# Performance work log

Hardware: AMD Instinct MI355X
Metric: run time of the kernel (lower is better)

The kernel has to match this reference:

```python
import jax, jax.numpy as jnp
import numpy as np

L, B, C_IN, C_OUT, C_COND, K, RATIO, TEMP = 1024, 8, 1024, 1024, 256, 4, 4, 30.0
HID = C_COND // RATIO


def setup_inputs() -> dict:
    key = jax.random.key(0)
    ks = jax.random.split(key, 8)
    s_in = 1.0 / np.sqrt(C_IN)
    s_cond = 1.0 / np.sqrt(C_COND)
    s_hid = 1.0 / np.sqrt(HID)
    return {
        "x": jax.random.normal(ks[0], (L, B, C_IN), jnp.float32),
        "cond": jax.random.normal(ks[1], (B, C_COND), jnp.float32),
        "fc1_w": jax.random.normal(ks[2], (HID, C_COND), jnp.float32) * s_cond,
        "fc1_b": jnp.zeros((HID,), jnp.float32),
        "fc2_w": jax.random.normal(ks[3], (K, HID), jnp.float32) * s_hid,
        "fc2_b": jnp.zeros((K,), jnp.float32),
        "weight": jax.random.normal(ks[4], (K, C_OUT, C_IN), jnp.float32) * s_in,
        "bias": jax.random.normal(ks[5], (K, C_OUT), jnp.float32) * s_in,
    }


def reference(x, cond, fc1_w, fc1_b, fc2_w, fc2_b, weight, bias):
    # attention over K experts, conditioned on style vector: (B, K)
    h = jax.nn.relu(cond @ fc1_w.T + fc1_b)
    att = jax.nn.softmax((h @ fc2_w.T + fc2_b) / TEMP, axis=-1)
    # per-sample aggregated weights: (B, C_out, C_in) and bias (B, C_out)
    w_b = jnp.einsum("bk,koi->boi", att, weight)
    b_b = att @ bias
    # grouped 1x1 conv == per-sample linear over the L dim: (L, B, C_out)
    out = jnp.einsum("lbi,boi->lbo", x, w_b) + b_b[None, :, :]
    return out
```

## Files before the change

### kernel.cpp

```cpp
#include <hip/hip_runtime.h>
#include <stdint.h>

#define L_DIM 1024
#define B_DIM 8
#define CIN   1024
#define COUT  1024
#define CCOND 256
#define KEXP  4
#define HID_DIM 64
#define TEMP_INV (1.0f/30.0f)

typedef float  f32x4 __attribute__((ext_vector_type(4)));
typedef __bf16 bf16x8 __attribute__((ext_vector_type(8)));

__device__ __forceinline__ ushort f2bf(float f) {
  union { float f; uint32_t u; } a; a.f = f;
  return (ushort)((a.u + 0x7fffu + ((a.u >> 16) & 1u)) >> 16);
}

__global__ __launch_bounds__(256) void prep_kernel(
                            const float* __restrict__ x,
                            const float* __restrict__ cond,
                            const float* __restrict__ fc1_w,
                            const float* __restrict__ fc1_b,
                            const float* __restrict__ fc2_w,
                            const float* __restrict__ fc2_b,
                            const float* __restrict__ bias,
                            ushort* __restrict__ xt,
                            float* __restrict__ att_out,
                            float* __restrict__ bb_out) {
  const int t = threadIdx.x;
  if (blockIdx.x == 0) {
    __shared__ float wlds[HID_DIM][CCOND + 4];
    __shared__ float clds[B_DIM][CCOND];
    __shared__ float h[B_DIM][HID_DIM];
    __shared__ float att[B_DIM][KEXP];
    #pragma unroll
    for (int ci = 0; ci < 16; ++ci) {
      int gi = ci * 256 + t;
      f32x4 v = ((const f32x4*)fc1_w)[gi];
      int j = gi >> 6, c4 = gi & 63;
      *(f32x4*)&wlds[j][c4 * 4] = v;
    }
    #pragma unroll
    for (int ci = 0; ci < 2; ++ci) {
      int gi = ci * 256 + t;
      ((f32x4*)clds)[gi] = ((const f32x4*)cond)[gi];
    }
    __syncthreads();
    {
      const int j = t & 63, b0 = t >> 6;
      float a0 = 0.f, a1 = 0.f;
      #pragma unroll 8
      for (int c4 = 0; c4 < 64; ++c4) {
        f32x4 wv = *(const f32x4*)&wlds[j][c4 * 4];
        f32x4 ca = *(const f32x4*)&clds[b0][c4 * 4];
        f32x4 cb = *(const f32x4*)&clds[b0 + 4][c4 * 4];
        a0 += wv.x*ca.x + wv.y*ca.y + wv.z*ca.z + wv.w*ca.w;
        a1 += wv.x*cb.x + wv.y*cb.y + wv.z*cb.z + wv.w*cb.w;
      }
      float bj = fc1_b[j];
      h[b0][j]     = fmaxf(a0 + bj, 0.0f);
      h[b0 + 4][j] = fmaxf(a1 + bj, 0.0f);
    }
    __syncthreads();
    if (t < B_DIM * KEXP) {
      const int b = t >> 2, k = t & 3;
      const float* wp = fc2_w + k * HID_DIM;
      float s = fc2_b[k];
      #pragma unroll 8
      for (int j = 0; j < HID_DIM; ++j) s = fmaf(h[b][j], wp[j], s);
      att[b][k] = s * TEMP_INV;
    }
    __syncthreads();
    if (t < B_DIM) {
      const int b = t;
      float m = fmaxf(fmaxf(att[b][0], att[b][1]), fmaxf(att[b][2], att[b][3]));
      float e0 = expf(att[b][0] - m), e1 = expf(att[b][1] - m);
      float e2 = expf(att[b][2] - m), e3 = expf(att[b][3] - m);
      float inv = 1.0f / (e0 + e1 + e2 + e3);
      att[b][0] = e0 * inv; att[b][1] = e1 * inv;
      att[b][2] = e2 * inv; att[b][3] = e3 * inv;
      att_out[b*KEXP+0] = att[b][0]; att_out[b*KEXP+1] = att[b][1];
      att_out[b*KEXP+2] = att[b][2]; att_out[b*KEXP+3] = att[b][3];
    }
    __syncthreads();
    for (int idx = t; idx < B_DIM * COUT; idx += 256) {
      const int b = idx >> 10, o = idx & (COUT - 1);
      float s = att[b][0] * bias[o]        + att[b][1] * bias[COUT + o]
              + att[b][2] * bias[2*COUT+o] + att[b][3] * bias[3*COUT+o];
      bb_out[idx] = s;
    }
  } else {
    const int C4 = CIN / 4;
    const int r0 = (blockIdx.x - 1) * 8;
    const f32x4* xp = (const f32x4*)x;
    f32x4 v[8];
    #pragma unroll
    for (int i = 0; i < 8; ++i)
      v[i] = xp[(size_t)(r0 + i) * C4 + t];
    #pragma unroll
    for (int i = 0; i < 8; ++i) {
      const int r = r0 + i;
      const int b = r & (B_DIM - 1);
      const int l = r >> 3;
      ushort4 o;
      o.x = f2bf(v[i].x); o.y = f2bf(v[i].y); o.z = f2bf(v[i].z); o.w = f2bf(v[i].w);
      ((ushort4*)xt)[(b * L_DIM + l) * C4 + t] = o;
    }
  }
}

__global__ void wmix_kernel(const float* __restrict__ weight,
                            const float* __restrict__ att,
                            ushort* __restrict__ wbb) {
  __shared__ float satt[B_DIM * KEXP];
  if (threadIdx.x < B_DIM * KEXP) satt[threadIdx.x] = att[threadIdx.x];
  __syncthreads();
  const int total4 = COUT * CIN / 4;
  int idx = blockIdx.x * blockDim.x + threadIdx.x;
  if (idx >= total4) return;
  f32x4 w0 = ((const f32x4*)weight)[idx];
  f32x4 w1 = ((const f32x4*)weight)[total4 + idx];
  f32x4 w2 = ((const f32x4*)weight)[2 * total4 + idx];
  f32x4 w3 = ((const f32x4*)weight)[3 * total4 + idx];
  #pragma unroll
  for (int b = 0; b < B_DIM; ++b) {
    f32x4 s = satt[b*4+0] * w0 + satt[b*4+1] * w1 + satt[b*4+2] * w2 + satt[b*4+3] * w3;
    ushort4 o;
    o.x = f2bf(s.x); o.y = f2bf(s.y); o.z = f2bf(s.z); o.w = f2bf(s.w);
    ((ushort4*)wbb)[b * total4 + idx] = o;
  }
}

#define GBM 256
#define GBN 128
#define GBK 64
#define GKT (CIN / GBK)

__global__ __launch_bounds__(512, 1) void gemm_kernel(
    const ushort* __restrict__ xt,
    const ushort* __restrict__ wbb,
    const float* __restrict__ bb,
    float* __restrict__ out)
{
  __shared__ ushort lds[3][(GBM + GBN) * GBK];

  const int bid = blockIdx.x;
  const int b  = bid & 7;
  const int tl = bid >> 3;
  const int mt = tl >> 3;
  const int nt = tl & 7;

  const int t = threadIdx.x;
  const int lane = t & 63;
  const int wid = t >> 6;
  const int wm = wid >> 1;
  const int wn = wid & 1;

  const ushort* __restrict__ Ag = xt  + (b * L_DIM + mt * GBM) * CIN;
  const ushort* __restrict__ Bg = wbb + (b * COUT  + nt * GBN) * CIN;

  const int srow = t >> 3;
  const int sg = (t & 7) ^ (srow & 7);

  f32x4 acc[4][4] = {};

  auto stage = [&](int bf, int kt) {
    #pragma unroll
    for (int i = 0; i < 4; ++i) {
      const int r = i * 64 + srow;
      __builtin_amdgcn_global_load_lds(
        (const __attribute__((address_space(1))) uint32_t*)(Ag + r * CIN + kt * GBK + sg * 8),
        (__attribute__((address_space(3))) uint32_t*)(&lds[bf][i * 4096 + t * 8]), 16, 0, 0);
    }
    #pragma unroll
    for (int i = 0; i < 2; ++i) {
      const int r = i * 64 + srow;
      __builtin_amdgcn_global_load_lds(
        (const __attribute__((address_space(1))) uint32_t*)(Bg + r * CIN + kt * GBK + sg * 8),
        (__attribute__((address_space(3))) uint32_t*)(&lds[bf][GBM * GBK + i * 4096 + t * 8]), 16, 0, 0);
    }
  };

  stage(0, 0);
  stage(1, 1);

  const int kg = lane >> 4;
  const int rr = lane & 15;

  #pragma unroll
  for (int kt = 0; kt < GKT; ++kt) {
    if (kt < GKT - 1) { asm volatile("s_waitcnt vmcnt(6)" ::: "memory"); }
    else              { asm volatile("s_waitcnt vmcnt(0)" ::: "memory"); }
    __builtin_amdgcn_sched_barrier(0);
    __builtin_amdgcn_s_barrier();
    __builtin_amdgcn_sched_barrier(0);
    if (kt + 2 < GKT) stage((kt + 2) % 3, kt + 2);
    __builtin_amdgcn_sched_barrier(0);

    const ushort* Ab = &lds[kt % 3][0];
    const ushort* Bb = &lds[kt % 3][GBM * GBK];
    bf16x8 af[4][2], bfv[4][2];
    #pragma unroll
    for (int kk = 0; kk < 2; ++kk) {
      const int sl = ((kk << 2) | kg) ^ (rr & 7);
      #pragma unroll
      for (int m = 0; m < 4; ++m)
        af[m][kk] = *(const bf16x8*)(Ab + (wm * 64 + m * 16 + rr) * GBK + sl * 8);
      #pragma unroll
      for (int n = 0; n < 4; ++n)
        bfv[n][kk] = *(const bf16x8*)(Bb + (wn * 64 + n * 16 + rr) * GBK + sl * 8);
    }
    __builtin_amdgcn_s_setprio(1);
    #pragma unroll
    for (int kk = 0; kk < 2; ++kk)
      #pragma unroll
      for (int m = 0; m < 4; ++m)
        #pragma unroll
        for (int n = 0; n < 4; ++n)
          acc[m][n] = __builtin_amdgcn_mfma_f32_16x16x32_bf16(af[m][kk], bfv[n][kk], acc[m][n], 0, 0, 0);
    __builtin_amdgcn_s_setprio(0);
  }

  const int colbase = nt * GBN + wn * 64;
  const int rowbase = mt * GBM + wm * 64;
  float bcol[4];
  #pragma unroll
  for (int n = 0; n < 4; ++n) bcol[n] = bb[b * COUT + colbase + n * 16 + rr];
  #pragma unroll
  for (int m = 0; m < 4; ++m) {
    #pragma unroll
    for (int j = 0; j < 4; ++j) {
      int row = rowbase + m * 16 + kg * 4 + j;
      float* op = out + row * (B_DIM * COUT) + b * COUT + colbase;
      #pragma unroll
      for (int n = 0; n < 4; ++n)
        op[n * 16 + rr] = acc[m][n][j] + bcol[n];
    }
  }
}

extern "C" void kernel_launch(void* const* d_in, const int* in_sizes, int n_in,
                              void* d_out, int out_size, void* d_ws, size_t ws_size,
                              hipStream_t stream) {
  const float* x      = (const float*)d_in[0];
  const float* cond   = (const float*)d_in[1];
  const float* fc1_w  = (const float*)d_in[2];
  const float* fc1_b  = (const float*)d_in[3];
  const float* fc2_w  = (const float*)d_in[4];
  const float* fc2_b  = (const float*)d_in[5];
  const float* weight = (const float*)d_in[6];
  const float* bias   = (const float*)d_in[7];
  float* out = (float*)d_out;

  char* ws = (char*)d_ws;
  float*  att = (float*)ws;
  float*  bbp = (float*)(ws + 256);
  ushort* xt  = (ushort*)(ws + 65536);
  ushort* wbb = (ushort*)(ws + 65536 + (size_t)L_DIM * B_DIM * CIN * 2);

  hipLaunchKernelGGL(prep_kernel, dim3(1 + (L_DIM * B_DIM) / 8), dim3(256), 0, stream,
                     x, cond, fc1_w, fc1_b, fc2_w, fc2_b, bias, xt, att, bbp);
  hipLaunchKernelGGL(wmix_kernel, dim3((COUT * CIN / 4) / 256), dim3(256), 0, stream,
                     weight, att, wbb);
  hipLaunchKernelGGL(gemm_kernel, dim3(B_DIM * (L_DIM / GBM) * (COUT / GBN)), dim3(512), 0, stream,
                     xt, wbb, bbp, out);
}
```

Measured before the change: 46.57 us.

## Fuse x fp32-to-bf16 conversion into GEMM A-tile loading via registers

```diff
diff --git a/kernel.cpp b/kernel.cpp
--- a/kernel.cpp
+++ b/kernel.cpp
@@ -18,96 +18,81 @@
   return (ushort)((a.u + 0x7fffu + ((a.u >> 16) & 1u)) >> 16);
 }
 
-__global__ __launch_bounds__(256) void prep_kernel(
-                            const float* __restrict__ x,
+__device__ __forceinline__ uint32_t cvtpk2(float a, float b) {
+  uint32_t r;
+  asm("v_cvt_pk_bf16_f32 %0, %1, %2" : "=v"(r) : "v"(a), "v"(b));
+  return r;
+}
+
+__global__ __launch_bounds__(256) void att_kernel(
                             const float* __restrict__ cond,
                             const float* __restrict__ fc1_w,
                             const float* __restrict__ fc1_b,
                             const float* __restrict__ fc2_w,
                             const float* __restrict__ fc2_b,
                             const float* __restrict__ bias,
-                            ushort* __restrict__ xt,
                             float* __restrict__ att_out,
                             float* __restrict__ bb_out) {
   const int t = threadIdx.x;
-  if (blockIdx.x == 0) {
-    __shared__ float wlds[HID_DIM][CCOND + 4];
-    __shared__ float clds[B_DIM][CCOND];
-    __shared__ float h[B_DIM][HID_DIM];
-    __shared__ float att[B_DIM][KEXP];
-    #pragma unroll
-    for (int ci = 0; ci < 16; ++ci) {
-      int gi = ci * 256 + t;
-      f32x4 v = ((const f32x4*)fc1_w)[gi];
-      int j = gi >> 6, c4 = gi & 63;
-      *(f32x4*)&wlds[j][c4 * 4] = v;
-    }
-    #pragma unroll
-    for (int ci = 0; ci < 2; ++ci) {
-      int gi = ci * 256 + t;
-      ((f32x4*)clds)[gi] = ((const f32x4*)cond)[gi];
-    }
-    __syncthreads();
-    {
-      const int j = t & 63, b0 = t >> 6;
-      float a0 = 0.f, a1 = 0.f;
-      #pragma unroll 8
-      for (int c4 = 0; c4 < 64; ++c4) {
-        f32x4 wv = *(const f32x4*)&wlds[j][c4 * 4];
-        f32x4 ca = *(const f32x4*)&clds[b0][c4 * 4];
-        f32x4 cb = *(const f32x4*)&clds[b0 + 4][c4 * 4];
-        a0 += wv.x*ca.x + wv.y*ca.y + wv.z*ca.z + wv.w*ca.w;
-        a1 += wv.x*cb.x + wv.y*cb.y + wv.z*cb.z + wv.w*cb.w;
-      }
-      float bj = fc1_b[j];
-      h[b0][j]     = fmaxf(a0 + bj, 0.0f);
-      h[b0 + 4][j] = fmaxf(a1 + bj, 0.0f);
-    }
-    __syncthreads();
-    if (t < B_DIM * KEXP) {
-      const int b = t >> 2, k = t & 3;
-      const float* wp = fc2_w + k * HID_DIM;
-      float s = fc2_b[k];
-      #pragma unroll 8
-      for (int j = 0; j < HID_DIM; ++j) s = fmaf(h[b][j], wp[j], s);
-      att[b][k] = s * TEMP_INV;
-    }
-    __syncthreads();
-    if (t < B_DIM) {
-      const int b = t;
-      float m = fmaxf(fmaxf(att[b][0], att[b][1]), fmaxf(att[b][2], att[b][3]));
-      float e0 = expf(att[b][0] - m), e1 = expf(att[b][1] - m);
-      float e2 = expf(att[b][2] - m), e3 = expf(att[b][3] - m);
-      float inv = 1.0f / (e0 + e1 + e2 + e3);
-      att[b][0] = e0 * inv; att[b][1] = e1 * inv;
-      att[b][2] = e2 * inv; att[b][3] = e3 * inv;
-      att_out[b*KEXP+0] = att[b][0]; att_out[b*KEXP+1] = att[b][1];
-      att_out[b*KEXP+2] = att[b][2]; att_out[b*KEXP+3] = att[b][3];
-    }
-    __syncthreads();
-    for (int idx = t; idx < B_DIM * COUT; idx += 256) {
-      const int b = idx >> 10, o = idx & (COUT - 1);
-      float s = att[b][0] * bias[o]        + att[b][1] * bias[COUT + o]
-              + att[b][2] * bias[2*COUT+o] + att[b][3] * bias[3*COUT+o];
-      bb_out[idx] = s;
-    }
-  } else {
-    const int C4 = CIN / 4;
-    const int r0 = (blockIdx.x - 1) * 8;
-    const f32x4* xp = (const f32x4*)x;
-    f32x4 v[8];
-    #pragma unroll
-    for (int i = 0; i < 8; ++i)
-      v[i] = xp[(size_t)(r0 + i) * C4 + t];
-    #pragma unroll
-    for (int i = 0; i < 8; ++i) {
-      const int r = r0 + i;
-      const int b = r & (B_DIM - 1);
-      const int l = r >> 3;
-      ushort4 o;
-      o.x = f2bf(v[i].x); o.y = f2bf(v[i].y); o.z = f2bf(v[i].z); o.w = f2bf(v[i].w);
-      ((ushort4*)xt)[(b * L_DIM + l) * C4 + t] = o;
-    }
+  __shared__ float wlds[HID_DIM][CCOND + 4];
+  __shared__ float clds[B_DIM][CCOND];
+  __shared__ float h[B_DIM][HID_DIM];
+  __shared__ float att[B_DIM][KEXP];
+  #pragma unroll
+  for (int ci = 0; ci < 16; ++ci) {
+    int gi = ci * 256 + t;
+    f32x4 v = ((const f32x4*)fc1_w)[gi];
+    int j = gi >> 6, c4 = gi & 63;
+    *(f32x4*)&wlds[j][c4 * 4] = v;
+  }
+  #pragma unroll
+  for (int ci = 0; ci < 2; ++ci) {
+    int gi = ci * 256 + t;
+    ((f32x4*)clds)[gi] = ((const f32x4*)cond)[gi];
+  }
+  __syncthreads();
+  {
+    const int j = t & 63, b0 = t >> 6;
+    float a0 = 0.f, a1 = 0.f;
+    #pragma unroll 8
+    for (int c4 = 0; c4 < 64; ++c4) {
+      f32x4 wv = *(const f32x4*)&wlds[j][c4 * 4];
+      f32x4 ca = *(const f32x4*)&clds[b0][c4 * 4];
+      f32x4 cb = *(const f32x4*)&clds[b0 + 4][c4 * 4];
+      a0 += wv.x*ca.x + wv.y*ca.y + wv.z*ca.z + wv.w*ca.w;
+      a1 += wv.x*cb.x + wv.y*cb.y + wv.z*cb.z + wv.w*cb.w;
+    }
+    float bj = fc1_b[j];
+    h[b0][j]     = fmaxf(a0 + bj, 0.0f);
+    h[b0 + 4][j] = fmaxf(a1 + bj, 0.0f);
+  }
+  __syncthreads();
+  if (t < B_DIM * KEXP) {
+    const int b = t >> 2, k = t & 3;
+    const float* wp = fc2_w + k * HID_DIM;
+    float s = fc2_b[k];
+    #pragma unroll 8
+    for (int j = 0; j < HID_DIM; ++j) s = fmaf(h[b][j], wp[j], s);
+    att[b][k] = s * TEMP_INV;
+  }
+  __syncthreads();
+  if (t < B_DIM) {
+    const int b = t;
+    float m = fmaxf(fmaxf(att[b][0], att[b][1]), fmaxf(att[b][2], att[b][3]));
+    float e0 = expf(att[b][0] - m), e1 = expf(att[b][1] - m);
+    float e2 = expf(att[b][2] - m), e3 = expf(att[b][3] - m);
+    float inv = 1.0f / (e0 + e1 + e2 + e3);
+    att[b][0] = e0 * inv; att[b][1] = e1 * inv;
+    att[b][2] = e2 * inv; att[b][3] = e3 * inv;
+    att_out[b*KEXP+0] = att[b][0]; att_out[b*KEXP+1] = att[b][1];
+    att_out[b*KEXP+2] = att[b][2]; att_out[b*KEXP+3] = att[b][3];
+  }
+  __syncthreads();
+  for (int idx = t; idx < B_DIM * COUT; idx += 256) {
+    const int b = idx >> 10, o = idx & (COUT - 1);
+    float s = att[b][0] * bias[o]        + att[b][1] * bias[COUT + o]
+            + att[b][2] * bias[2*COUT+o] + att[b][3] * bias[3*COUT+o];
+    bb_out[idx] = s;
   }
 }
 
@@ -139,8 +124,8 @@
 #define GKT (CIN / GBK)
 
 __global__ __launch_bounds__(512, 1) void gemm_kernel(
-    const ushort* __restrict__ xt,
     const ushort* __restrict__ wbb,
+    const float* __restrict__ x,
     const float* __restrict__ bb,
     float* __restrict__ out)
 {
@@ -158,22 +143,25 @@
   const int wm = wid >> 1;
   const int wn = wid & 1;
 
-  const ushort* __restrict__ Ag = xt  + (b * L_DIM + mt * GBM) * CIN;
-  const ushort* __restrict__ Bg = wbb + (b * COUT  + nt * GBN) * CIN;
+  const float*  __restrict__ Ag = x   + (size_t)(mt * GBM) * (B_DIM * CIN) + b * CIN;
+  const ushort* __restrict__ Bg = wbb + (b * COUT + nt * GBN) * CIN;
 
   const int srow = t >> 3;
   const int sg = (t & 7) ^ (srow & 7);
 
   f32x4 acc[4][4] = {};
-
-  auto stage = [&](int bf, int kt) {
+  f32x4 ra[4][2];
+
+  auto loadA = [&](int kt) {
     #pragma unroll
     for (int i = 0; i < 4; ++i) {
-      const int r = i * 64 + srow;
-      __builtin_amdgcn_global_load_lds(
-        (const __attribute__((address_space(1))) uint32_t*)(Ag + r * CIN + kt * GBK + sg * 8),
-        (__attribute__((address_space(3))) uint32_t*)(&lds[bf][i * 4096 + t * 8]), 16, 0, 0);
-    }
+      const float* p = Ag + (size_t)(i * 64 + srow) * (B_DIM * CIN) + kt * GBK + sg * 8;
+      ra[i][0] = *(const f32x4*)(p);
+      ra[i][1] = *(const f32x4*)(p + 4);
+    }
+    __builtin_amdgcn_sched_barrier(0);
+  };
+  auto loadB = [&](int bf, int kt) {
     #pragma unroll
     for (int i = 0; i < 2; ++i) {
       const int r = i * 64 + srow;
@@ -181,22 +169,41 @@
         (const __attribute__((address_space(1))) uint32_t*)(Bg + r * CIN + kt * GBK + sg * 8),
         (__attribute__((address_space(3))) uint32_t*)(&lds[bf][GBM * GBK + i * 4096 + t * 8]), 16, 0, 0);
     }
+    __builtin_amdgcn_sched_barrier(0);
   };
-
-  stage(0, 0);
-  stage(1, 1);
+  auto writeA = [&](int bf) {
+    #pragma unroll
+    for (int i = 0; i < 4; ++i) {
+      uint4 v;
+      v.x = cvtpk2(ra[i][0].x, ra[i][0].y);
+      v.y = cvtpk2(ra[i][0].z, ra[i][0].w);
+      v.z = cvtpk2(ra[i][1].x, ra[i][1].y);
+      v.w = cvtpk2(ra[i][1].z, ra[i][1].w);
+      *(uint4*)(&lds[bf][i * 4096 + t * 8]) = v;
+    }
+    __builtin_amdgcn_sched_barrier(0);
+  };
+
+  loadA(0);
+  loadB(0, 0);
+  asm volatile("s_waitcnt vmcnt(2)" ::: "memory");
+  writeA(0);
+  loadA(1);
+  loadB(1, 1);
 
   const int kg = lane >> 4;
   const int rr = lane & 15;
 
   #pragma unroll
   for (int kt = 0; kt < GKT; ++kt) {
-    if (kt < GKT - 1) { asm volatile("s_waitcnt vmcnt(6)" ::: "memory"); }
+    if (kt < GKT - 1) { asm volatile("s_waitcnt vmcnt(2)" ::: "memory"); }
     else              { asm volatile("s_waitcnt vmcnt(0)" ::: "memory"); }
+    asm volatile("s_waitcnt lgkmcnt(0)" ::: "memory");
     __builtin_amdgcn_sched_barrier(0);
     __builtin_amdgcn_s_barrier();
     __builtin_amdgcn_sched_barrier(0);
-    if (kt + 2 < GKT) stage((kt + 2) % 3, kt + 2);
+    if (kt + 1 < GKT) writeA((kt + 1) % 3);
+    if (kt + 2 < GKT) { loadA(kt + 2); loadB((kt + 2) % 3, kt + 2); }
     __builtin_amdgcn_sched_barrier(0);
 
     const ushort* Ab = &lds[kt % 3][0];
@@ -257,13 +264,12 @@
   char* ws = (char*)d_ws;
   float*  att = (float*)ws;
   float*  bbp = (float*)(ws + 256);
-  ushort* xt  = (ushort*)(ws + 65536);
-  ushort* wbb = (ushort*)(ws + 65536 + (size_t)L_DIM * B_DIM * CIN * 2);
-
-  hipLaunchKernelGGL(prep_kernel, dim3(1 + (L_DIM * B_DIM) / 8), dim3(256), 0, stream,
-                     x, cond, fc1_w, fc1_b, fc2_w, fc2_b, bias, xt, att, bbp);
+  ushort* wbb = (ushort*)(ws + 65536);
+
+  hipLaunchKernelGGL(att_kernel, dim3(1), dim3(256), 0, stream,
+                     cond, fc1_w, fc1_b, fc2_w, fc2_b, bias, att, bbp);
   hipLaunchKernelGGL(wmix_kernel, dim3((COUT * CIN / 4) / 256), dim3(256), 0, stream,
                      weight, att, wbb);
   hipLaunchKernelGGL(gemm_kernel, dim3(B_DIM * (L_DIM / GBM) * (COUT / GBN)), dim3(512), 0, stream,
-                     xt, wbb, bbp, out);
-}
+                     wbb, x, bbp, out);
+}
```

Result: slower. 49.96 us (+7.3%).

## Fuse weight mixing into prep kernel by recomputing attention per block

Applied to the files above, without the earlier changes.

```diff
diff --git a/kernel.cpp b/kernel.cpp
--- a/kernel.cpp
+++ b/kernel.cpp
@@ -18,82 +18,29 @@
   return (ushort)((a.u + 0x7fffu + ((a.u >> 16) & 1u)) >> 16);
 }
 
-__global__ __launch_bounds__(256) void prep_kernel(
+__global__ __launch_bounds__(256) void fused_prep_kernel(
                             const float* __restrict__ x,
                             const float* __restrict__ cond,
                             const float* __restrict__ fc1_w,
                             const float* __restrict__ fc1_b,
                             const float* __restrict__ fc2_w,
                             const float* __restrict__ fc2_b,
+                            const float* __restrict__ weight,
                             const float* __restrict__ bias,
                             ushort* __restrict__ xt,
-                            float* __restrict__ att_out,
+                            ushort* __restrict__ wbb,
                             float* __restrict__ bb_out) {
   const int t = threadIdx.x;
-  if (blockIdx.x == 0) {
-    __shared__ float wlds[HID_DIM][CCOND + 4];
-    __shared__ float clds[B_DIM][CCOND];
-    __shared__ float h[B_DIM][HID_DIM];
-    __shared__ float att[B_DIM][KEXP];
-    #pragma unroll
-    for (int ci = 0; ci < 16; ++ci) {
-      int gi = ci * 256 + t;
-      f32x4 v = ((const f32x4*)fc1_w)[gi];
-      int j = gi >> 6, c4 = gi & 63;
-      *(f32x4*)&wlds[j][c4 * 4] = v;
-    }
-    #pragma unroll
-    for (int ci = 0; ci < 2; ++ci) {
-      int gi = ci * 256 + t;
-      ((f32x4*)clds)[gi] = ((const f32x4*)cond)[gi];
-    }
-    __syncthreads();
-    {
-      const int j = t & 63, b0 = t >> 6;
-      float a0 = 0.f, a1 = 0.f;
-      #pragma unroll 8
-      for (int c4 = 0; c4 < 64; ++c4) {
-        f32x4 wv = *(const f32x4*)&wlds[j][c4 * 4];
-        f32x4 ca = *(const f32x4*)&clds[b0][c4 * 4];
-        f32x4 cb = *(const f32x4*)&clds[b0 + 4][c4 * 4];
-        a0 += wv.x*ca.x + wv.y*ca.y + wv.z*ca.z + wv.w*ca.w;
-        a1 += wv.x*cb.x + wv.y*cb.y + wv.z*cb.z + wv.w*cb.w;
-      }
-      float bj = fc1_b[j];
-      h[b0][j]     = fmaxf(a0 + bj, 0.0f);
-      h[b0 + 4][j] = fmaxf(a1 + bj, 0.0f);
-    }
-    __syncthreads();
-    if (t < B_DIM * KEXP) {
-      const int b = t >> 2, k = t & 3;
-      const float* wp = fc2_w + k * HID_DIM;
-      float s = fc2_b[k];
-      #pragma unroll 8
-      for (int j = 0; j < HID_DIM; ++j) s = fmaf(h[b][j], wp[j], s);
-      att[b][k] = s * TEMP_INV;
-    }
-    __syncthreads();
-    if (t < B_DIM) {
-      const int b = t;
-      float m = fmaxf(fmaxf(att[b][0], att[b][1]), fmaxf(att[b][2], att[b][3]));
-      float e0 = expf(att[b][0] - m), e1 = expf(att[b][1] - m);
-      float e2 = expf(att[b][2] - m), e3 = expf(att[b][3] - m);
-      float inv = 1.0f / (e0 + e1 + e2 + e3);
-      att[b][0] = e0 * inv; att[b][1] = e1 * inv;
-      att[b][2] = e2 * inv; att[b][3] = e3 * inv;
-      att_out[b*KEXP+0] = att[b][0]; att_out[b*KEXP+1] = att[b][1];
-      att_out[b*KEXP+2] = att[b][2]; att_out[b*KEXP+3] = att[b][3];
-    }
-    __syncthreads();
-    for (int idx = t; idx < B_DIM * COUT; idx += 256) {
-      const int b = idx >> 10, o = idx & (COUT - 1);
-      float s = att[b][0] * bias[o]        + att[b][1] * bias[COUT + o]
-              + att[b][2] * bias[2*COUT+o] + att[b][3] * bias[3*COUT+o];
-      bb_out[idx] = s;
-    }
-  } else {
+  __shared__ float wlds[HID_DIM][CCOND + 4];
+  __shared__ float clds[B_DIM][CCOND];
+  __shared__ float h[B_DIM][HID_DIM];
+  __shared__ float att[B_DIM][KEXP];
+
+  const int bid = blockIdx.x;
+
+  if (bid != 0 && ((bid - 1) & 1) == 0) {
     const int C4 = CIN / 4;
-    const int r0 = (blockIdx.x - 1) * 8;
+    const int r0 = ((bid - 1) >> 1) * 8;
     const f32x4* xp = (const f32x4*)x;
     f32x4 v[8];
     #pragma unroll
@@ -108,28 +55,86 @@
       o.x = f2bf(v[i].x); o.y = f2bf(v[i].y); o.z = f2bf(v[i].z); o.w = f2bf(v[i].w);
       ((ushort4*)xt)[(b * L_DIM + l) * C4 + t] = o;
     }
-  }
-}
-
-__global__ void wmix_kernel(const float* __restrict__ weight,
-                            const float* __restrict__ att,
-                            ushort* __restrict__ wbb) {
-  __shared__ float satt[B_DIM * KEXP];
-  if (threadIdx.x < B_DIM * KEXP) satt[threadIdx.x] = att[threadIdx.x];
-  __syncthreads();
+    return;
+  }
+
+  const bool is_wmix = (bid != 0);
   const int total4 = COUT * CIN / 4;
-  int idx = blockIdx.x * blockDim.x + threadIdx.x;
-  if (idx >= total4) return;
-  f32x4 w0 = ((const f32x4*)weight)[idx];
-  f32x4 w1 = ((const f32x4*)weight)[total4 + idx];
-  f32x4 w2 = ((const f32x4*)weight)[2 * total4 + idx];
-  f32x4 w3 = ((const f32x4*)weight)[3 * total4 + idx];
+  int widx = 0;
+  f32x4 w0, w1, w2, w3;
+  if (is_wmix) {
+    widx = ((bid - 1) >> 1) * 256 + t;
+    w0 = ((const f32x4*)weight)[widx];
+    w1 = ((const f32x4*)weight)[total4 + widx];
+    w2 = ((const f32x4*)weight)[2 * total4 + widx];
+    w3 = ((const f32x4*)weight)[3 * total4 + widx];
+  }
+
+  #pragma unroll
+  for (int ci = 0; ci < 16; ++ci) {
+    int gi = ci * 256 + t;
+    f32x4 v = ((const f32x4*)fc1_w)[gi];
+    int j = gi >> 6, c4 = gi & 63;
+    *(f32x4*)&wlds[j][c4 * 4] = v;
+  }
+  #pragma unroll
+  for (int ci = 0; ci < 2; ++ci) {
+    int gi = ci * 256 + t;
+    ((f32x4*)clds)[gi] = ((const f32x4*)cond)[gi];
+  }
+  __syncthreads();
+  {
+    const int j = t & 63, b0 = t >> 6;
+    float a0 = 0.f, a1 = 0.f;
+    #pragma unroll 8
+    for (int c4 = 0; c4 < 64; ++c4) {
+      f32x4 wv = *(const f32x4*)&wlds[j][c4 * 4];
+      f32x4 ca = *(const f32x4*)&clds[b0][c4 * 4];
+      f32x4 cb = *(const f32x4*)&clds[b0 + 4][c4 * 4];
+      a0 += wv.x*ca.x + wv.y*ca.y + wv.z*ca.z + wv.w*ca.w;
+      a1 += wv.x*cb.x + wv.y*cb.y + wv.z*cb.z + wv.w*cb.w;
+    }
+    float bj = fc1_b[j];
+    h[b0][j]     = fmaxf(a0 + bj, 0.0f);
+    h[b0 + 4][j] = fmaxf(a1 + bj, 0.0f);
+  }
+  __syncthreads();
+  if (t < B_DIM * KEXP) {
+    const int b = t >> 2, k = t & 3;
+    const float* wp = fc2_w + k * HID_DIM;
+    float s = fc2_b[k];
+    #pragma unroll 8
+    for (int j = 0; j < HID_DIM; ++j) s = fmaf(h[b][j], wp[j], s);
+    att[b][k] = s * TEMP_INV;
+  }
+  __syncthreads();
+  if (t < B_DIM) {
+    const int b = t;
+    float m = fmaxf(fmaxf(att[b][0], att[b][1]), fmaxf(att[b][2], att[b][3]));
+    float e0 = expf(att[b][0] - m), e1 = expf(att[b][1] - m);
+    float e2 = expf(att[b][2] - m), e3 = expf(att[b][3] - m);
+    float inv = 1.0f / (e0 + e1 + e2 + e3);
+    att[b][0] = e0 * inv; att[b][1] = e1 * inv;
+    att[b][2] = e2 * inv; att[b][3] = e3 * inv;
+  }
+  __syncthreads();
+
+  if (!is_wmix) {
+    for (int idx = t; idx < B_DIM * COUT; idx += 256) {
+      const int b = idx >> 10, o = idx & (COUT - 1);
+      float s = att[b][0] * bias[o]        + att[b][1] * bias[COUT + o]
+              + att[b][2] * bias[2*COUT+o] + att[b][3] * bias[3*COUT+o];
+      bb_out[idx] = s;
+    }
+    return;
+  }
+
   #pragma unroll
   for (int b = 0; b < B_DIM; ++b) {
-    f32x4 s = satt[b*4+0] * w0 + satt[b*4+1] * w1 + satt[b*4+2] * w2 + satt[b*4+3] * w3;
+    f32x4 s = att[b][0] * w0 + att[b][1] * w1 + att[b][2] * w2 + att[b][3] * w3;
     ushort4 o;
     o.x = f2bf(s.x); o.y = f2bf(s.y); o.z = f2bf(s.z); o.w = f2bf(s.w);
-    ((ushort4*)wbb)[b * total4 + idx] = o;
+    ((ushort4*)wbb)[b * total4 + widx] = o;
   }
 }
 
@@ -255,15 +260,12 @@
   float* out = (float*)d_out;
 
   char* ws = (char*)d_ws;
-  float*  att = (float*)ws;
   float*  bbp = (float*)(ws + 256);
   ushort* xt  = (ushort*)(ws + 65536);
   ushort* wbb = (ushort*)(ws + 65536 + (size_t)L_DIM * B_DIM * CIN * 2);
 
-  hipLaunchKernelGGL(prep_kernel, dim3(1 + (L_DIM * B_DIM) / 8), dim3(256), 0, stream,
-                     x, cond, fc1_w, fc1_b, fc2_w, fc2_b, bias, xt, att, bbp);
-  hipLaunchKernelGGL(wmix_kernel, dim3((COUT * CIN / 4) / 256), dim3(256), 0, stream,
-                     weight, att, wbb);
+  hipLaunchKernelGGL(fused_prep_kernel, dim3(1 + 2 * 1024), dim3(256), 0, stream,
+                     x, cond, fc1_w, fc1_b, fc2_w, fc2_b, weight, bias, xt, wbb, bbp);
   hipLaunchKernelGGL(gemm_kernel, dim3(B_DIM * (L_DIM / GBM) * (COUT / GBN)), dim3(512), 0, stream,
                      xt, wbb, bbp, out);
 }
```

Result: slower. 60.73 us (+30.4%).

## Split attention into tiny kernel and fuse x-transpose with weight mixing

Applied to the files above, without the earlier changes.

```diff
diff --git a/kernel.cpp b/kernel.cpp
--- a/kernel.cpp
+++ b/kernel.cpp
@@ -18,82 +18,85 @@
   return (ushort)((a.u + 0x7fffu + ((a.u >> 16) & 1u)) >> 16);
 }
 
-__global__ __launch_bounds__(256) void prep_kernel(
-                            const float* __restrict__ x,
+__global__ __launch_bounds__(256) void att_kernel(
                             const float* __restrict__ cond,
                             const float* __restrict__ fc1_w,
                             const float* __restrict__ fc1_b,
                             const float* __restrict__ fc2_w,
                             const float* __restrict__ fc2_b,
                             const float* __restrict__ bias,
-                            ushort* __restrict__ xt,
                             float* __restrict__ att_out,
                             float* __restrict__ bb_out) {
   const int t = threadIdx.x;
-  if (blockIdx.x == 0) {
-    __shared__ float wlds[HID_DIM][CCOND + 4];
-    __shared__ float clds[B_DIM][CCOND];
-    __shared__ float h[B_DIM][HID_DIM];
-    __shared__ float att[B_DIM][KEXP];
-    #pragma unroll
-    for (int ci = 0; ci < 16; ++ci) {
-      int gi = ci * 256 + t;
-      f32x4 v = ((const f32x4*)fc1_w)[gi];
-      int j = gi >> 6, c4 = gi & 63;
-      *(f32x4*)&wlds[j][c4 * 4] = v;
-    }
-    #pragma unroll
-    for (int ci = 0; ci < 2; ++ci) {
-      int gi = ci * 256 + t;
-      ((f32x4*)clds)[gi] = ((const f32x4*)cond)[gi];
-    }
-    __syncthreads();
-    {
-      const int j = t & 63, b0 = t >> 6;
-      float a0 = 0.f, a1 = 0.f;
-      #pragma unroll 8
-      for (int c4 = 0; c4 < 64; ++c4) {
-        f32x4 wv = *(const f32x4*)&wlds[j][c4 * 4];
-        f32x4 ca = *(const f32x4*)&clds[b0][c4 * 4];
-        f32x4 cb = *(const f32x4*)&clds[b0 + 4][c4 * 4];
-        a0 += wv.x*ca.x + wv.y*ca.y + wv.z*ca.z + wv.w*ca.w;
-        a1 += wv.x*cb.x + wv.y*cb.y + wv.z*cb.z + wv.w*cb.w;
-      }
-      float bj = fc1_b[j];
-      h[b0][j]     = fmaxf(a0 + bj, 0.0f);
-      h[b0 + 4][j] = fmaxf(a1 + bj, 0.0f);
-    }
-    __syncthreads();
-    if (t < B_DIM * KEXP) {
-      const int b = t >> 2, k = t & 3;
-      const float* wp = fc2_w + k * HID_DIM;
-      float s = fc2_b[k];
-      #pragma unroll 8
-      for (int j = 0; j < HID_DIM; ++j) s = fmaf(h[b][j], wp[j], s);
-      att[b][k] = s * TEMP_INV;
-    }
-    __syncthreads();
-    if (t < B_DIM) {
-      const int b = t;
-      float m = fmaxf(fmaxf(att[b][0], att[b][1]), fmaxf(att[b][2], att[b][3]));
-      float e0 = expf(att[b][0] - m), e1 = expf(att[b][1] - m);
-      float e2 = expf(att[b][2] - m), e3 = expf(att[b][3] - m);
-      float inv = 1.0f / (e0 + e1 + e2 + e3);
-      att[b][0] = e0 * inv; att[b][1] = e1 * inv;
-      att[b][2] = e2 * inv; att[b][3] = e3 * inv;
-      att_out[b*KEXP+0] = att[b][0]; att_out[b*KEXP+1] = att[b][1];
-      att_out[b*KEXP+2] = att[b][2]; att_out[b*KEXP+3] = att[b][3];
-    }
-    __syncthreads();
-    for (int idx = t; idx < B_DIM * COUT; idx += 256) {
-      const int b = idx >> 10, o = idx & (COUT - 1);
-      float s = att[b][0] * bias[o]        + att[b][1] * bias[COUT + o]
-              + att[b][2] * bias[2*COUT+o] + att[b][3] * bias[3*COUT+o];
-      bb_out[idx] = s;
-    }
-  } else {
+  __shared__ float clds[B_DIM][CCOND];
+  __shared__ float h[B_DIM][HID_DIM];
+  __shared__ float att[B_DIM][KEXP];
+  #pragma unroll
+  for (int ci = 0; ci < 2; ++ci) {
+    int gi = ci * 256 + t;
+    ((f32x4*)clds)[gi] = ((const f32x4*)cond)[gi];
+  }
+  __syncthreads();
+  {
+    const int j = t & 63, b0 = t >> 6;
+    const f32x4* wrow = ((const f32x4*)fc1_w) + j * 64;
+    float a0 = 0.f, a1 = 0.f;
+    #pragma unroll 8
+    for (int c4 = 0; c4 < 64; ++c4) {
+      f32x4 wv = wrow[c4];
+      f32x4 ca = *(const f32x4*)&clds[b0][c4 * 4];
+      f32x4 cb = *(const f32x4*)&clds[b0 + 4][c4 * 4];
+      a0 += wv.x*ca.x + wv.y*ca.y + wv.z*ca.z + wv.w*ca.w;
+      a1 += wv.x*cb.x + wv.y*cb.y + wv.z*cb.z + wv.w*cb.w;
+    }
+    float bj = fc1_b[j];
+    h[b0][j]     = fmaxf(a0 + bj, 0.0f);
+    h[b0 + 4][j] = fmaxf(a1 + bj, 0.0f);
+  }
+  __syncthreads();
+  if (t < B_DIM * KEXP) {
+    const int b = t >> 2, k = t & 3;
+    const float* wp = fc2_w + k * HID_DIM;
+    float s = fc2_b[k];
+    #pragma unroll 8
+    for (int j = 0; j < HID_DIM; ++j) s = fmaf(h[b][j], wp[j], s);
+    att[b][k] = s * TEMP_INV;
+  }
+  __syncthreads();
+  if (t < B_DIM) {
+    const int b = t;
+    float m = fmaxf(fmaxf(att[b][0], att[b][1]), fmaxf(att[b][2], att[b][3]));
+    float e0 = expf(att[b][0] - m), e1 = expf(att[b][1] - m);
+    float e2 = expf(att[b][2] - m), e3 = expf(att[b][3] - m);
+    float inv = 1.0f / (e0 + e1 + e2 + e3);
+    att[b][0] = e0 * inv; att[b][1] = e1 * inv;
+    att[b][2] = e2 * inv; att[b][3] = e3 * inv;
+    att_out[b*KEXP+0] = att[b][0]; att_out[b*KEXP+1] = att[b][1];
+    att_out[b*KEXP+2] = att[b][2]; att_out[b*KEXP+3] = att[b][3];
+  }
+  __syncthreads();
+  for (int idx = t; idx < B_DIM * COUT; idx += 256) {
+    const int b = idx >> 10, o = idx & (COUT - 1);
+    float s = att[b][0] * bias[o]        + att[b][1] * bias[COUT + o]
+            + att[b][2] * bias[2*COUT+o] + att[b][3] * bias[3*COUT+o];
+    bb_out[idx] = s;
+  }
+}
+
+__global__ __launch_bounds__(256) void stream_kernel(
+                            const float* __restrict__ x,
+                            const float* __restrict__ weight,
+                            const float* __restrict__ att,
+                            ushort* __restrict__ xt,
+                            ushort* __restrict__ wbb) {
+  const int t = threadIdx.x;
+  const int bid = blockIdx.x;
+  __shared__ float satt[B_DIM * KEXP];
+
+  if (bid % 5 != 0) {
+    const int xb = bid - 1 - bid / 5;
     const int C4 = CIN / 4;
-    const int r0 = (blockIdx.x - 1) * 8;
+    const int r0 = xb * 8;
     const f32x4* xp = (const f32x4*)x;
     f32x4 v[8];
     #pragma unroll
@@ -108,28 +111,28 @@
       o.x = f2bf(v[i].x); o.y = f2bf(v[i].y); o.z = f2bf(v[i].z); o.w = f2bf(v[i].w);
       ((ushort4*)xt)[(b * L_DIM + l) * C4 + t] = o;
     }
-  }
-}
-
-__global__ void wmix_kernel(const float* __restrict__ weight,
-                            const float* __restrict__ att,
-                            ushort* __restrict__ wbb) {
-  __shared__ float satt[B_DIM * KEXP];
-  if (threadIdx.x < B_DIM * KEXP) satt[threadIdx.x] = att[threadIdx.x];
-  __syncthreads();
+    return;
+  }
+
+  const int wb = bid / 5;
   const int total4 = COUT * CIN / 4;
-  int idx = blockIdx.x * blockDim.x + threadIdx.x;
-  if (idx >= total4) return;
-  f32x4 w0 = ((const f32x4*)weight)[idx];
-  f32x4 w1 = ((const f32x4*)weight)[total4 + idx];
-  f32x4 w2 = ((const f32x4*)weight)[2 * total4 + idx];
-  f32x4 w3 = ((const f32x4*)weight)[3 * total4 + idx];
-  #pragma unroll
-  for (int b = 0; b < B_DIM; ++b) {
-    f32x4 s = satt[b*4+0] * w0 + satt[b*4+1] * w1 + satt[b*4+2] * w2 + satt[b*4+3] * w3;
-    ushort4 o;
-    o.x = f2bf(s.x); o.y = f2bf(s.y); o.z = f2bf(s.z); o.w = f2bf(s.w);
-    ((ushort4*)wbb)[b * total4 + idx] = o;
+  const int base = wb * 1024 + t;
+  if (t < B_DIM * KEXP) satt[t] = att[t];
+  __syncthreads();
+  #pragma unroll
+  for (int c = 0; c < 4; ++c) {
+    const int idx = base + c * 256;
+    f32x4 w0 = ((const f32x4*)weight)[idx];
+    f32x4 w1 = ((const f32x4*)weight)[total4 + idx];
+    f32x4 w2 = ((const f32x4*)weight)[2 * total4 + idx];
+    f32x4 w3 = ((const f32x4*)weight)[3 * total4 + idx];
+    #pragma unroll
+    for (int b = 0; b < B_DIM; ++b) {
+      f32x4 s = satt[b*4+0] * w0 + satt[b*4+1] * w1 + satt[b*4+2] * w2 + satt[b*4+3] * w3;
+      ushort4 o;
+      o.x = f2bf(s.x); o.y = f2bf(s.y); o.z = f2bf(s.z); o.w = f2bf(s.w);
+      ((ushort4*)wbb)[b * total4 + idx] = o;
+    }
   }
 }
 
@@ -260,10 +263,10 @@
   ushort* xt  = (ushort*)(ws + 65536);
   ushort* wbb = (ushort*)(ws + 65536 + (size_t)L_DIM * B_DIM * CIN * 2);
 
-  hipLaunchKernelGGL(prep_kernel, dim3(1 + (L_DIM * B_DIM) / 8), dim3(256), 0, stream,
-                     x, cond, fc1_w, fc1_b, fc2_w, fc2_b, bias, xt, att, bbp);
-  hipLaunchKernelGGL(wmix_kernel, dim3((COUT * CIN / 4) / 256), dim3(256), 0, stream,
-                     weight, att, wbb);
+  hipLaunchKernelGGL(att_kernel, dim3(1), dim3(256), 0, stream,
+                     cond, fc1_w, fc1_b, fc2_w, fc2_b, bias, att, bbp);
+  hipLaunchKernelGGL(stream_kernel, dim3(1280), dim3(256), 0, stream,
+                     x, weight, att, xt, wbb);
   hipLaunchKernelGGL(gemm_kernel, dim3(B_DIM * (L_DIM / GBM) * (COUT / GBN)), dim3(512), 0, stream,
                      xt, wbb, bbp, out);
 }
```

Result: slower. 58.90 us (+26.5%).
